# Performance work log

Measured on AMD Instinct MI355X. Metric: run time of the kernel, lower is better.

The kernel has to match this reference:

```python
import jax, jax.numpy as jnp
import numpy as np

B, Q, K, C, H = 64, 512, 512, 256, 8
HD = C // H  # per-head dim = 32
OUT = 256


def setup_inputs() -> dict:
    key = jax.random.key(0)
    ks = jax.random.split(key, 11)
    s = 0.05
    return {
        "q_data": jax.random.normal(ks[0], (B, Q, C), jnp.float32),
        "m_data": jax.random.normal(ks[1], (B, K, C), jnp.float32),
        "bias": jax.random.normal(ks[2], (B, 1, Q, K), jnp.float32),
        "nonbatched_bias": jax.random.normal(ks[3], (H, Q, K), jnp.float32),
        "query_w": jax.random.normal(ks[4], (C, H, HD), jnp.float32) * s,
        "key_w": jax.random.normal(ks[5], (C, H, HD), jnp.float32) * s,
        "value_w": jax.random.normal(ks[6], (C, H, HD), jnp.float32) * s,
        "gating_w": jax.random.normal(ks[7], (C, H, HD), jnp.float32) * s,
        "gating_b": jnp.ones((H, HD), jnp.float32),
        "output_w": jax.random.normal(ks[8], (H, HD, OUT), jnp.float32) * s,
        "output_b": jnp.zeros((OUT,), jnp.float32),
    }


def reference(q_data, m_data, bias, nonbatched_bias, query_w, key_w, value_w,
              gating_w, gating_b, output_w, output_b):
    key_dim = query_w.shape[-1]
    # projections
    q = jnp.einsum('bqa,ahc->bqhc', q_data, query_w) * key_dim ** (-0.5)
    k = jnp.einsum('bka,ahc->bkhc', m_data, key_w)
    v = jnp.einsum('bka,ahc->bkhc', m_data, value_w)
    # bias-augmented attention logits [b,h,q,k]
    logits = jnp.einsum('bqhc,bkhc->bhqk', q, k) + bias
    logits = logits + nonbatched_bias[None]
    weights = jax.nn.softmax(logits, axis=-1)
    weighted_avg = jnp.einsum('bhqk,bkhc->bqhc', weights, v)
    # sigmoid gating
    gate = jax.nn.sigmoid(jnp.einsum('bqc,chv->bqhv', q_data, gating_w) + gating_b)
    weighted_avg = weighted_avg * gate
    # output projection
    return jnp.einsum('bqhc,hco->bqo', weighted_avg, output_w) + output_b
```

## Files before the change

kernel.cpp:

```cpp
#include <hip/hip_runtime.h>
#include <math.h>

#define Bb 64
#define Qn 512
#define Kn 512
#define Cn 256
#define Hn 8
#define HDn 32
#define OUTn 256

typedef __bf16 bf16_t;
typedef __attribute__((ext_vector_type(4))) __bf16 bf16x4;
typedef __attribute__((ext_vector_type(8))) __bf16 bf16x8;
typedef __attribute__((ext_vector_type(4))) float f32x4;
typedef __attribute__((ext_vector_type(4))) unsigned int u32x4;

__device__ inline bf16_t tob(float f) {
    unsigned int u = __float_as_uint(f);
    u += 0x7fff + ((u >> 16) & 1);
    unsigned short s = (unsigned short)(u >> 16);
    return __builtin_bit_cast(bf16_t, s);
}

__device__ inline void gl_lds16(const void* g, void* l) {
    __builtin_amdgcn_global_load_lds(
        (const __attribute__((address_space(1))) unsigned int*)g,
        (__attribute__((address_space(3))) unsigned int*)l, 16, 0, 0);
}

__global__ __launch_bounds__(256) void prep_weights(
    const float* __restrict__ qw, const float* __restrict__ kw,
    const float* __restrict__ vw, const float* __restrict__ gw,
    const float* __restrict__ ow,
    bf16_t* __restrict__ wtq, bf16_t* __restrict__ wtk,
    bf16_t* __restrict__ wtv, bf16_t* __restrict__ wtg,
    bf16_t* __restrict__ wto)
{
    int tid = blockIdx.x * 256 + threadIdx.x;
    int mat = tid >> 16;
    int rem = tid & 65535;
    int a = rem >> 8;
    int n = rem & 255;
    const float* src = mat == 0 ? qw : mat == 1 ? kw : mat == 2 ? vw : mat == 3 ? gw : ow;
    bf16_t* dst = mat == 0 ? wtq : mat == 1 ? wtk : mat == 2 ? wtv : mat == 3 ? wtg : wto;
    int nb = n >> 4, kb = a >> 5, rg = (a >> 3) & 3, e = a & 7, nl = n & 15;
    size_t idx = (((size_t)(nb * 8 + kb) * 64) + rg * 16 + nl) * 8 + e;
    dst[idx] = tob(src[a * 256 + n]);
}

__global__ __launch_bounds__(256) void prep_bias(
    const float* __restrict__ bias, const float* __restrict__ nbias,
    float* __restrict__ btile, float* __restrict__ ntile)
{
    size_t vid = (size_t)blockIdx.x * 256 + threadIdx.x;
    const size_t NB = (size_t)64 * 65536;
    int lane, t, c, q16;
    if (vid < NB) {
        lane = vid & 63; t = (vid >> 6) & 3; c = (vid >> 8) & 7; q16 = (vid >> 11) & 31;
        int b = vid >> 16;
        int row = q16 * 16 + (lane & 15);
        int col = c * 64 + t * 16 + (lane >> 4) * 4;
        f32x4 v = *reinterpret_cast<const f32x4*>(bias + ((size_t)b * Qn + row) * Kn + col);
        *reinterpret_cast<f32x4*>(btile + vid * 4) = v;
    } else {
        size_t nv = vid - NB;
        lane = nv & 63; t = (nv >> 6) & 3; c = (nv >> 8) & 7; q16 = (nv >> 11) & 31;
        int h = nv >> 16;
        int row = q16 * 16 + (lane & 15);
        int col = c * 64 + t * 16 + (lane >> 4) * 4;
        f32x4 v = *reinterpret_cast<const f32x4*>(nbias + ((size_t)h * Qn + row) * Kn + col);
        *reinterpret_cast<f32x4*>(ntile + nv * 4) = v;
    }
}

#define ALDS_STRIDE 264
__global__ __launch_bounds__(512) void proj_kernel(
    const float* __restrict__ qdata, const float* __restrict__ mdata,
    const bf16_t* __restrict__ wtq, const bf16_t* __restrict__ wtk,
    const bf16_t* __restrict__ wtv, const bf16_t* __restrict__ wtg,
    const float* __restrict__ gating_b,
    bf16_t* __restrict__ qb, bf16_t* __restrict__ kb,
    bf16_t* __restrict__ vTb, bf16_t* __restrict__ gateb)
{
    __shared__ __align__(16) bf16_t smem[20480];
    bf16_t* alds = smem;
    const int side = blockIdx.y;
    const int m0 = blockIdx.x * 64;
    const int tid = threadIdx.x;
    const int lane = tid & 63;
    const int w = tid >> 6;
    const int ch = w >> 2;
    const int ncb = (w & 3) * 64;
    const int c15 = lane & 15;
    const int rgrp = lane >> 4;
    const int kof = rgrp * 8;
    const float* X = side ? mdata : qdata;
    const bf16_t* Wt = side == 0 ? (ch == 0 ? wtq : wtg) : (ch == 0 ? wtk : wtv);
    const bool vout = (side == 1) && (ch == 1);

    #pragma unroll
    for (int i = 0; i < 8; i++) {
        int u = tid + i * 512;
        int row = u >> 6;
        int c4 = u & 63;
        f32x4 a4 = *reinterpret_cast<const f32x4*>(X + (size_t)(m0 + row) * 256 + c4 * 4);
        unsigned int p0, p1;
        asm("v_cvt_pk_bf16_f32 %0, %1, %2" : "=v"(p0) : "v"(a4[0]), "v"(a4[1]));
        asm("v_cvt_pk_bf16_f32 %0, %1, %2" : "=v"(p1) : "v"(a4[2]), "v"(a4[3]));
        unsigned long long pk = ((unsigned long long)p1 << 32) | p0;
        *reinterpret_cast<unsigned long long*>(&alds[row * ALDS_STRIDE + c4 * 4]) = pk;
    }
    __syncthreads();

    const bf16_t* wbase = Wt + (size_t)(ncb >> 4) * 8 * 512 + lane * 8;
    f32x4 acc[4][4] = {};
    #pragma unroll
    for (int kc = 0; kc < 8; kc++) {
        bf16x8 am[4], bn[4];
        #pragma unroll
        for (int i = 0; i < 4; i++)
            am[i] = *reinterpret_cast<const bf16x8*>(&alds[(i * 16 + c15) * ALDS_STRIDE + kc * 32 + kof]);
        #pragma unroll
        for (int j = 0; j < 4; j++)
            bn[j] = *reinterpret_cast<const bf16x8*>(wbase + ((size_t)j * 8 + kc) * 512);
        #pragma unroll
        for (int i = 0; i < 4; i++)
            #pragma unroll
            for (int j = 0; j < 4; j++) {
                if (vout)
                    acc[i][j] = __builtin_amdgcn_mfma_f32_16x16x32_bf16(bn[j], am[i], acc[i][j], 0, 0, 0);
                else
                    acc[i][j] = __builtin_amdgcn_mfma_f32_16x16x32_bf16(am[i], bn[j], acc[i][j], 0, 0, 0);
            }
    }

    __syncthreads();
    bf16_t* scr = smem + w * 2560;

    const float scale = 0.17677669529663687f * 1.4426950408889634f;
    const int hbase = ncb >> 5;
    const int posbase = m0 & 511;
    const int b = m0 >> 9;

    if (!vout) {
        bf16_t* dst = side == 0 ? (ch == 0 ? qb : gateb) : kb;
        #pragma unroll
        for (int P = 0; P < 2; P++) {
            #pragma unroll
            for (int ii = 0; ii < 2; ii++) {
                int i = P * 2 + ii;
                #pragma unroll
                for (int j = 0; j < 4; j++) {
                    int n = ncb + j * 16 + c15;
                    #pragma unroll
                    for (int r = 0; r < 4; r++) {
                        float v = acc[i][j][r];
                        if (side == 0) {
                            if (ch == 0) v *= scale;
                            else v = 1.f / (1.f + __expf(-(v + gating_b[n])));
                        }
                        scr[(ii * 16 + rgrp * 4 + r) * 72 + j * 16 + c15] = tob(v);
                    }
                }
            }
            asm volatile("" ::: "memory");
            #pragma unroll
            for (int v2 = 0; v2 < 4; v2++) {
                int row = v2 * 8 + (lane >> 3);
                int col = (lane & 7) * 8;
                bf16x8 val = *reinterpret_cast<const bf16x8*>(&scr[row * 72 + col]);
                int pos = posbase + P * 32 + row;
                int hh = hbase + (col >> 5);
                int d = col & 31;
                *reinterpret_cast<bf16x8*>(dst + (((size_t)(b * Hn + hh) * Qn + pos) << 5) + d) = val;
            }
            asm volatile("" ::: "memory");
        }
    } else {
        #pragma unroll
        for (int P = 0; P < 2; P++) {
            #pragma unroll
            for (int ii = 0; ii < 2; ii++) {
                int i = P * 2 + ii;
                int kperm = (((c15 >> 3) & 1) << 4) | (((c15 >> 2) & 1) << 3) | (ii << 2)
                          | (((c15 >> 1) & 1) << 1) | (c15 & 1);
                #pragma unroll
                for (int j = 0; j < 4; j++)
                    #pragma unroll
                    for (int r = 0; r < 4; r++)
                        scr[(j * 16 + rgrp * 4 + r) * 40 + kperm] = tob(acc[i][j][r]);
            }
            asm volatile("" ::: "memory");
            #pragma unroll
            for (int u = 0; u < 4; u++) {
                int nloc = u * 16 + (lane >> 2);
                int koff = (lane & 3) * 8;
                bf16x8 val = *reinterpret_cast<const bf16x8*>(&scr[nloc * 40 + koff]);
                int hh = hbase + (nloc >> 5);
                int d = nloc & 31;
                *reinterpret_cast<bf16x8*>(vTb + ((size_t)(b * Hn + hh) * HDn + d) * Kn
                                           + posbase + P * 32 + koff) = val;
            }
            asm volatile("" ::: "memory");
        }
    }
}

__global__ __launch_bounds__(256) void attn_kernel(
    const bf16_t* __restrict__ qb, const bf16_t* __restrict__ kb,
    const bf16_t* __restrict__ vTb, const bf16_t* __restrict__ gateb,
    const float* __restrict__ btile, const float* __restrict__ ntile,
    bf16_t* __restrict__ wab)
{
    __shared__ __align__(16) char kvlds[2][8192];
    const int p = blockIdx.x;
    const int qt = p & 7;
    const int h = (p >> 3) & 7;
    const int b = p >> 6;
    const int lane = threadIdx.x & 63;
    const int wv = threadIdx.x >> 6;
    const int q0 = qt * 64 + wv * 16;
    const int q16 = qt * 4 + wv;
    const int c15 = lane & 15;
    const int rgrp = lane >> 4;
    const int kof = rgrp * 8;

    const bf16_t* qbase = qb + (size_t)(b * Hn + h) * Qn * HDn;
    const bf16_t* kbase = kb + (size_t)(b * Hn + h) * Kn * HDn;
    const bf16_t* vbase = vTb + (size_t)(b * Hn + h) * HDn * Kn;
    const float* btb = btile + (((size_t)b * 32 + q16) << 13) + lane * 4;
    const float* ntb = ntile + (((size_t)h * 32 + q16) << 13) + lane * 4;

    const int krw = (wv << 4) + (lane >> 2);
    const int kcb = (lane & 3) << 4;
    const int vrw = (wv << 3) + (lane >> 3);
    const int vcb = (lane & 7) << 4;
    const size_t ksrc0 = ((size_t)krw << 6) + (size_t)(kcb ^ ((krw & 3) << 4));
    const size_t vsrc0 = ((size_t)vrw << 10) + (size_t)(vcb ^ ((vrw & 7) << 4));

    bf16x8 aq = *reinterpret_cast<const bf16x8*>(qbase + (q0 + c15) * HDn + kof);

    const float NML = -12.f * 1.4426950408889634f;
    const float LOG2E = 1.4426950408889634f;
    const f32x4 zML = {NML, NML, NML, NML};
    f32x4 o[2] = {};
    f32x4 lsv = {0.f, 0.f, 0.f, 0.f};

    gl_lds16((const char*)kbase + ksrc0, (char*)kvlds[0] + wv * 1024);
    gl_lds16((const char*)vbase + vsrc0, (char*)kvlds[0] + 4096 + wv * 1024);

    #pragma unroll 1
    for (int c = 0; c < 8; c++) {
        const int pb = c & 1;
        f32x4 bt[4], nt_[4];
        #pragma unroll
        for (int t = 0; t < 4; t++) {
            bt[t]  = *reinterpret_cast<const f32x4*>(btb + c * 1024 + t * 256);
            nt_[t] = *reinterpret_cast<const f32x4*>(ntb + c * 1024 + t * 256);
        }
        __builtin_amdgcn_sched_barrier(0);
        asm volatile("s_waitcnt vmcnt(8)" ::: "memory");
        __builtin_amdgcn_s_barrier();
        __builtin_amdgcn_sched_barrier(0);
        if (c < 7) {
            char* dstb = (char*)kvlds[pb ^ 1] + wv * 1024;
            gl_lds16((const char*)kbase + (size_t)((c + 1) << 12) + ksrc0, dstb);
            gl_lds16((const char*)vbase + (size_t)((c + 1) << 7) + vsrc0, dstb + 4096);
        }
        const char* kl = (const char*)kvlds[pb];
        f32x4 sc[4];
        #pragma unroll
        for (int t = 0; t < 4; t++) {
            int kr = t * 16 + c15;
            bf16x8 kf = *reinterpret_cast<const bf16x8*>(kl + (kr << 6) + ((rgrp << 4) ^ ((kr & 3) << 4)));
            sc[t] = __builtin_amdgcn_mfma_f32_16x16x32_bf16(kf, aq, zML, 0, 0, 0);
        }
        f32x4 es[4];
        #pragma unroll
        for (int t = 0; t < 4; t++) {
            f32x4 bb = bt[t] + nt_[t];
            #pragma unroll
            for (int r = 0; r < 4; r++)
                es[t][r] = __builtin_amdgcn_exp2f(fmaf(bb[r], LOG2E, sc[t][r]));
            lsv += es[t];
        }
        unsigned int pw[8];
        #pragma unroll
        for (int t = 0; t < 4; t++) {
            asm("v_cvt_pk_bf16_f32 %0, %1, %2" : "=v"(pw[t * 2 + 0]) : "v"(es[t][0]), "v"(es[t][1]));
            asm("v_cvt_pk_bf16_f32 %0, %1, %2" : "=v"(pw[t * 2 + 1]) : "v"(es[t][2]), "v"(es[t][3]));
        }
        u32x4 a0 = {pw[0], pw[1], pw[2], pw[3]};
        u32x4 a1 = {pw[4], pw[5], pw[6], pw[7]};
        bf16x8 pa0 = __builtin_bit_cast(bf16x8, a0);
        bf16x8 pa1 = __builtin_bit_cast(bf16x8, a1);
        #pragma unroll
        for (int sub = 0; sub < 2; sub++) {
            bf16x8 ap = sub == 0 ? pa0 : pa1;
            #pragma unroll
            for (int nt = 0; nt < 2; nt++) {
                int vr = nt * 16 + c15;
                bf16x8 bv = *reinterpret_cast<const bf16x8*>(kl + 4096 + (vr << 7)
                                + (((sub << 6) | (rgrp << 4)) ^ ((vr & 7) << 4)));
                o[nt] = __builtin_amdgcn_mfma_f32_16x16x32_bf16(ap, bv, o[nt], 0, 0, 0);
            }
        }
    }

    float lsum = (lsv[0] + lsv[1]) + (lsv[2] + lsv[3]);
    lsum += __shfl_xor(lsum, 16, 64);
    lsum += __shfl_xor(lsum, 32, 64);
    float linv[4];
    #pragma unroll
    for (int r = 0; r < 4; r++)
        linv[r] = 1.f / __shfl(lsum, rgrp * 4 + r, 64);

    const bf16_t* gptr = gateb + (size_t)(b * Hn + h) * Qn * HDn;
    bf16_t* wptr = wab + (size_t)b * Qn * 256;
    const int qg = q0 + rgrp * 4;
    #pragma unroll
    for (int nt = 0; nt < 2; nt++) {
        int d = nt * 16 + c15;
        #pragma unroll
        for (int r = 0; r < 4; r++) {
            float g = (float)gptr[(qg + r) * HDn + d];
            wptr[(qg + r) * 256 + h * 32 + d] = tob(o[nt][r] * linv[r] * g);
        }
    }
}

__global__ __launch_bounds__(256) void outproj_kernel(
    const bf16_t* __restrict__ wab, const bf16_t* __restrict__ wto,
    const float* __restrict__ outb, float* __restrict__ out)
{
    __shared__ bf16_t alds[64 * ALDS_STRIDE];
    const int m0 = blockIdx.x * 64;
    const int tid = threadIdx.x;
    const int lane = tid & 63;
    const int w = tid >> 6;
    const int ncb = w * 64;
    const int c15 = lane & 15;
    const int rgrp = lane >> 4;
    const int kof = rgrp * 8;

    #pragma unroll
    for (int i = 0; i < 8; i++) {
        int u = tid + i * 256;
        int row = u >> 5;
        int c16 = u & 31;
        bf16x8 a8 = *reinterpret_cast<const bf16x8*>(wab + (size_t)(m0 + row) * 256 + c16 * 8);
        *reinterpret_cast<bf16x8*>(&alds[row * ALDS_STRIDE + c16 * 8]) = a8;
    }
    __syncthreads();

    const bf16_t* wbase = wto + (size_t)(ncb >> 4) * 8 * 512 + lane * 8;
    f32x4 acc[4][4] = {};
    #pragma unroll
    for (int kc = 0; kc < 8; kc++) {
        bf16x8 am[4], bn[4];
        #pragma unroll
        for (int i = 0; i < 4; i++)
            am[i] = *reinterpret_cast<const bf16x8*>(&alds[(i * 16 + c15) * ALDS_STRIDE + kc * 32 + kof]);
        #pragma unroll
        for (int j = 0; j < 4; j++)
            bn[j] = *reinterpret_cast<const bf16x8*>(wbase + ((size_t)j * 8 + kc) * 512);
        #pragma unroll
        for (int i = 0; i < 4; i++)
            #pragma unroll
            for (int j = 0; j < 4; j++)
                acc[i][j] = __builtin_amdgcn_mfma_f32_16x16x32_bf16(am[i], bn[j], acc[i][j], 0, 0, 0);
    }

    #pragma unroll
    for (int j = 0; j < 4; j++) {
        int n = ncb + j * 16 + c15;
        float ob = outb[n];
        #pragma unroll
        for (int i = 0; i < 4; i++) {
            #pragma unroll
            for (int r = 0; r < 4; r++) {
                int m = m0 + i * 16 + rgrp * 4 + r;
                out[(size_t)m * 256 + n] = acc[i][j][r] + ob;
            }
        }
    }
}

extern "C" void kernel_launch(void* const* d_in, const int* in_sizes, int n_in,
                              void* d_out, int out_size, void* d_ws, size_t ws_size,
                              hipStream_t stream) {
    const float* q_data = (const float*)d_in[0];
    const float* m_data = (const float*)d_in[1];
    const float* bias = (const float*)d_in[2];
    const float* nbias = (const float*)d_in[3];
    const float* query_w = (const float*)d_in[4];
    const float* key_w = (const float*)d_in[5];
    const float* value_w = (const float*)d_in[6];
    const float* gating_w = (const float*)d_in[7];
    const float* gating_b = (const float*)d_in[8];
    const float* output_w = (const float*)d_in[9];
    const float* output_b = (const float*)d_in[10];
    float* out = (float*)d_out;

    char* ws = (char*)d_ws;
    const size_t WT = 256 * 256 * sizeof(bf16_t);
    const size_t PROJ = (size_t)Bb * Hn * Qn * HDn;
    bf16_t* wtq = (bf16_t*)(ws);
    bf16_t* wtk = (bf16_t*)(ws + WT);
    bf16_t* wtv = (bf16_t*)(ws + 2 * WT);
    bf16_t* wtg = (bf16_t*)(ws + 3 * WT);
    bf16_t* wto = (bf16_t*)(ws + 4 * WT);
    bf16_t* qb = (bf16_t*)(ws + 5 * WT);
    bf16_t* kb = qb + PROJ;
    bf16_t* vtb = kb + PROJ;
    bf16_t* gateb = vtb + PROJ;
    bf16_t* wab = gateb + PROJ;

    const size_t BASE = 5 * WT + 5 * PROJ * sizeof(bf16_t);
    const size_t BT_BYTES = (size_t)64 * 65536 * 16;
    float* btile = (float*)(ws + BASE);
    float* ntile = (float*)(ws + BASE + BT_BYTES);

    prep_weights<<<1280, 256, 0, stream>>>(query_w, key_w, value_w, gating_w, output_w,
                                           wtq, wtk, wtv, wtg, wto);
    prep_bias<<<18432, 256, 0, stream>>>(bias, nbias, btile, ntile);
    proj_kernel<<<dim3(512, 2), 512, 0, stream>>>(q_data, m_data, wtq, wtk, wtv, wtg,
                                                  gating_b, qb, kb, vtb, gateb);
    attn_kernel<<<4096, 256, 0, stream>>>(qb, kb, vtb, gateb, btile, ntile, wab);
    outproj_kernel<<<512, 256, 0, stream>>>(wab, wto, output_b, out);
}
```

Before: 174.1 us.

## Split projection kernel into smaller per-matrix blocks for higher occupancy

The projection kernel is re-gridded from 1024 blocks of 512 threads, each covering 64 rows and two weight matrices, to 4096 blocks of 256 threads, each covering 32 rows and one matrix. Per-wave accumulators shrink and the LDS footprint halves, with launch bounds asking for 8 blocks per CU so more waves can hide memory latency. In exchange each input tile is loaded and converted to bf16 four times instead of twice. The k-loop is also no longer unrolled.

```diff
diff --git a/kernel.cpp b/kernel.cpp
--- a/kernel.cpp
+++ b/kernel.cpp
@@ -74,7 +74,7 @@
 }
 
 #define ALDS_STRIDE 264
-__global__ __launch_bounds__(512) void proj_kernel(
+__global__ __launch_bounds__(256, 8) void proj_kernel(
     const float* __restrict__ qdata, const float* __restrict__ mdata,
     const bf16_t* __restrict__ wtq, const bf16_t* __restrict__ wtk,
     const bf16_t* __restrict__ wtv, const bf16_t* __restrict__ wtg,
@@ -82,25 +82,24 @@
     bf16_t* __restrict__ qb, bf16_t* __restrict__ kb,
     bf16_t* __restrict__ vTb, bf16_t* __restrict__ gateb)
 {
-    __shared__ __align__(16) bf16_t smem[20480];
+    __shared__ __align__(16) bf16_t smem[10304];
     bf16_t* alds = smem;
-    const int side = blockIdx.y;
-    const int m0 = blockIdx.x * 64;
+    const int mat = blockIdx.y;
+    const int m0 = blockIdx.x * 32;
     const int tid = threadIdx.x;
     const int lane = tid & 63;
     const int w = tid >> 6;
-    const int ch = w >> 2;
-    const int ncb = (w & 3) * 64;
+    const int ncb = w * 64;
     const int c15 = lane & 15;
     const int rgrp = lane >> 4;
     const int kof = rgrp * 8;
-    const float* X = side ? mdata : qdata;
-    const bf16_t* Wt = side == 0 ? (ch == 0 ? wtq : wtg) : (ch == 0 ? wtk : wtv);
-    const bool vout = (side == 1) && (ch == 1);
+    const float* X = (mat == 0 || mat == 3) ? qdata : mdata;
+    const bf16_t* Wt = mat == 0 ? wtq : mat == 1 ? wtk : mat == 2 ? wtv : wtg;
+    const bool vout = (mat == 2);
 
     #pragma unroll
     for (int i = 0; i < 8; i++) {
-        int u = tid + i * 512;
+        int u = tid + i * 256;
         int row = u >> 6;
         int c4 = u & 63;
         f32x4 a4 = *reinterpret_cast<const f32x4*>(X + (size_t)(m0 + row) * 256 + c4 * 4);
@@ -113,18 +112,18 @@
     __syncthreads();
 
     const bf16_t* wbase = Wt + (size_t)(ncb >> 4) * 8 * 512 + lane * 8;
-    f32x4 acc[4][4] = {};
-    #pragma unroll
+    f32x4 acc[2][4] = {};
+    #pragma unroll 1
     for (int kc = 0; kc < 8; kc++) {
-        bf16x8 am[4], bn[4];
-        #pragma unroll
-        for (int i = 0; i < 4; i++)
+        bf16x8 am[2], bn[4];
+        #pragma unroll
+        for (int i = 0; i < 2; i++)
             am[i] = *reinterpret_cast<const bf16x8*>(&alds[(i * 16 + c15) * ALDS_STRIDE + kc * 32 + kof]);
         #pragma unroll
         for (int j = 0; j < 4; j++)
             bn[j] = *reinterpret_cast<const bf16x8*>(wbase + ((size_t)j * 8 + kc) * 512);
         #pragma unroll
-        for (int i = 0; i < 4; i++)
+        for (int i = 0; i < 2; i++)
             #pragma unroll
             for (int j = 0; j < 4; j++) {
                 if (vout)
@@ -135,7 +134,7 @@
     }
 
     __syncthreads();
-    bf16_t* scr = smem + w * 2560;
+    bf16_t* scr = smem + w * 2576;
 
     const float scale = 0.17677669529663687f * 1.4426950408889634f;
     const int hbase = ncb >> 5;
@@ -143,65 +142,51 @@
     const int b = m0 >> 9;
 
     if (!vout) {
-        bf16_t* dst = side == 0 ? (ch == 0 ? qb : gateb) : kb;
-        #pragma unroll
-        for (int P = 0; P < 2; P++) {
-            #pragma unroll
-            for (int ii = 0; ii < 2; ii++) {
-                int i = P * 2 + ii;
+        bf16_t* dst = mat == 0 ? qb : mat == 1 ? kb : gateb;
+        #pragma unroll
+        for (int i = 0; i < 2; i++)
+            #pragma unroll
+            for (int j = 0; j < 4; j++) {
+                int n_loc = j * 16 + c15;
                 #pragma unroll
-                for (int j = 0; j < 4; j++) {
-                    int n = ncb + j * 16 + c15;
-                    #pragma unroll
-                    for (int r = 0; r < 4; r++) {
-                        float v = acc[i][j][r];
-                        if (side == 0) {
-                            if (ch == 0) v *= scale;
-                            else v = 1.f / (1.f + __expf(-(v + gating_b[n])));
-                        }
-                        scr[(ii * 16 + rgrp * 4 + r) * 72 + j * 16 + c15] = tob(v);
-                    }
+                for (int r = 0; r < 4; r++) {
+                    float v = acc[i][j][r];
+                    if (mat == 0) v *= scale;
+                    else if (mat == 3) v = 1.f / (1.f + __expf(-(v + gating_b[ncb + n_loc])));
+                    scr[(i * 16 + rgrp * 4 + r) * 72 + n_loc] = tob(v);
                 }
             }
-            asm volatile("" ::: "memory");
-            #pragma unroll
-            for (int v2 = 0; v2 < 4; v2++) {
-                int row = v2 * 8 + (lane >> 3);
-                int col = (lane & 7) * 8;
-                bf16x8 val = *reinterpret_cast<const bf16x8*>(&scr[row * 72 + col]);
-                int pos = posbase + P * 32 + row;
-                int hh = hbase + (col >> 5);
-                int d = col & 31;
-                *reinterpret_cast<bf16x8*>(dst + (((size_t)(b * Hn + hh) * Qn + pos) << 5) + d) = val;
-            }
-            asm volatile("" ::: "memory");
+        asm volatile("" ::: "memory");
+        #pragma unroll
+        for (int u = 0; u < 4; u++) {
+            int row = u * 8 + (lane >> 3);
+            int nof = (lane & 7) * 8;
+            bf16x8 val = *reinterpret_cast<const bf16x8*>(&scr[row * 72 + nof]);
+            int hh = hbase + (nof >> 5);
+            int d = nof & 31;
+            int pos = posbase + row;
+            *reinterpret_cast<bf16x8*>(dst + (((size_t)(b * Hn + hh) * Qn + pos) << 5) + d) = val;
         }
     } else {
         #pragma unroll
-        for (int P = 0; P < 2; P++) {
-            #pragma unroll
-            for (int ii = 0; ii < 2; ii++) {
-                int i = P * 2 + ii;
-                int kperm = (((c15 >> 3) & 1) << 4) | (((c15 >> 2) & 1) << 3) | (ii << 2)
-                          | (((c15 >> 1) & 1) << 1) | (c15 & 1);
+        for (int i = 0; i < 2; i++) {
+            int col = (((c15 >> 3) & 1) << 4) | (((c15 >> 2) & 1) << 3) | (i << 2) | (c15 & 3);
+            #pragma unroll
+            for (int j = 0; j < 4; j++)
                 #pragma unroll
-                for (int j = 0; j < 4; j++)
-                    #pragma unroll
-                    for (int r = 0; r < 4; r++)
-                        scr[(j * 16 + rgrp * 4 + r) * 40 + kperm] = tob(acc[i][j][r]);
-            }
-            asm volatile("" ::: "memory");
-            #pragma unroll
-            for (int u = 0; u < 4; u++) {
-                int nloc = u * 16 + (lane >> 2);
-                int koff = (lane & 3) * 8;
-                bf16x8 val = *reinterpret_cast<const bf16x8*>(&scr[nloc * 40 + koff]);
-                int hh = hbase + (nloc >> 5);
-                int d = nloc & 31;
-                *reinterpret_cast<bf16x8*>(vTb + ((size_t)(b * Hn + hh) * HDn + d) * Kn
-                                           + posbase + P * 32 + koff) = val;
-            }
-            asm volatile("" ::: "memory");
+                for (int r = 0; r < 4; r++)
+                    scr[(j * 16 + rgrp * 4 + r) * 40 + col] = tob(acc[i][j][r]);
+        }
+        asm volatile("" ::: "memory");
+        #pragma unroll
+        for (int u = 0; u < 4; u++) {
+            int n_loc = u * 16 + (lane >> 2);
+            int mof = (lane & 3) * 8;
+            bf16x8 val = *reinterpret_cast<const bf16x8*>(&scr[n_loc * 40 + mof]);
+            int hh = hbase + (n_loc >> 5);
+            int d = n_loc & 31;
+            *reinterpret_cast<bf16x8*>(vTb + ((size_t)(b * Hn + hh) * HDn + d) * Kn
+                                       + posbase + mof) = val;
         }
     }
 }
@@ -424,8 +409,8 @@
     prep_weights<<<1280, 256, 0, stream>>>(query_w, key_w, value_w, gating_w, output_w,
                                            wtq, wtk, wtv, wtg, wto);
     prep_bias<<<18432, 256, 0, stream>>>(bias, nbias, btile, ntile);
-    proj_kernel<<<dim3(512, 2), 512, 0, stream>>>(q_data, m_data, wtq, wtk, wtv, wtg,
-                                                  gating_b, qb, kb, vtb, gateb);
+    proj_kernel<<<dim3(1024, 4), 256, 0, stream>>>(q_data, m_data, wtq, wtk, wtv, wtg,
+                                                   gating_b, qb, kb, vtb, gateb);
     attn_kernel<<<4096, 256, 0, stream>>>(qb, kb, vtb, gateb, btile, ntile, wab);
     outproj_kernel<<<512, 256, 0, stream>>>(wab, wto, output_b, out);
 }
```

Result: slower. 198.9 us (+14.2%).
